# Kernel tuning notes

Hardware: AMD Instinct MI355X
Metric: run time of the kernel (lower is better)

Reference implementation:

```python
import jax, jax.numpy as jnp
import numpy as np

STRIDE = (1, 1)
PAD = (1, 1)
DIL = (1, 1)
KH, KW = 3, 3
DEFORM_GROUPS = 2


def setup_inputs() -> dict:
    key = jax.random.key(0)
    ks = jax.random.split(key, 5)
    B, C, H, W = 4, 128, 64, 64
    Cout = 128
    K = KH * KW
    n = C * KH * KW
    stdv = 1.0 / np.sqrt(n)
    x = jax.random.normal(ks[0], (B, C, H, W), dtype=jnp.float32)
    offset = jax.random.normal(ks[1], (B, DEFORM_GROUPS * 2 * K, H, W), dtype=jnp.float32)
    mask = jax.random.uniform(ks[2], (B, DEFORM_GROUPS * K, H, W), dtype=jnp.float32)
    weight = jax.random.uniform(ks[3], (Cout, C, KH, KW), minval=-stdv, maxval=stdv, dtype=jnp.float32)
    bias = jnp.zeros((Cout,), dtype=jnp.float32)
    return {"x": x, "offset": offset, "mask": mask, "weight": weight, "bias": bias}


def _mdcn_forward(x, offset, mask, weight, bias):
    B, C, H, W = x.shape
    Cout, Cin_g, kh, kw = weight.shape
    K = kh * kw
    dg = offset.shape[1] // (2 * K)
    Cg = C // dg
    sh, sw = STRIDE
    ph, pw = PAD
    dh, dw = DIL
    Ho = (H + 2 * ph - (dh * (kh - 1) + 1)) // sh + 1
    Wo = (W + 2 * pw - (dw * (kw - 1) + 1)) // sw + 1

    # offsets: (B, dg, K, 2, Ho, Wo) with (dy, dx) pairs; mask: (B, dg, K, Ho, Wo)
    off = offset.reshape(B, dg, K, 2, Ho, Wo)
    m = mask.reshape(B, dg, K, Ho, Wo)

    ky, kx = jnp.meshgrid(jnp.arange(kh), jnp.arange(kw), indexing="ij")
    ky = ky.reshape(K).astype(x.dtype)  # kernel tap row offsets
    kx = kx.reshape(K).astype(x.dtype)
    oy = (jnp.arange(Ho) * sh - ph).astype(x.dtype)
    ox = (jnp.arange(Wo) * sw - pw).astype(x.dtype)

    # sampling positions (B, dg, K, Ho, Wo)
    py = off[:, :, :, 0] + oy[None, None, None, :, None] + (ky * dh)[None, None, :, None, None]
    px = off[:, :, :, 1] + ox[None, None, None, None, :] + (kx * dw)[None, None, :, None, None]

    y0 = jnp.floor(py)
    x0 = jnp.floor(px)
    ly = py - y0
    lx = px - x0
    y0i = y0.astype(jnp.int32)
    x0i = x0.astype(jnp.int32)

    xg = x.reshape(B, dg, Cg, H * W)

    def gather(yi, xi):
        valid = (yi >= 0) & (yi < H) & (xi >= 0) & (xi < W)
        idx = jnp.clip(yi, 0, H - 1) * W + jnp.clip(xi, 0, W - 1)  # (B,dg,K,Ho,Wo)
        g = jax.vmap(jax.vmap(lambda xf, ix: xf[:, ix]))(xg, idx.reshape(B, dg, K * Ho * Wo))
        g = g.reshape(B, dg, Cg, K, Ho, Wo)
        return g * valid[:, :, None].astype(x.dtype)

    w00 = ((1 - ly) * (1 - lx))[:, :, None]
    w01 = ((1 - ly) * lx)[:, :, None]
    w10 = (ly * (1 - lx))[:, :, None]
    w11 = (ly * lx)[:, :, None]

    val = (w00 * gather(y0i, x0i)
           + w01 * gather(y0i, x0i + 1)
           + w10 * gather(y0i + 1, x0i)
           + w11 * gather(y0i + 1, x0i + 1))

    # modulation and im2col-GEMM (groups=1): col (B, C*K, Ho*Wo)
    col = (val * m[:, :, None]).reshape(B, C * K, Ho * Wo)
    wk = weight.reshape(Cout, C * K)
    out = jnp.einsum("ok,bkp->bop", wk, col).reshape(B, Cout, Ho, Wo)
    return out + bias[None, :, None, None]


def reference(x, offset, mask, weight, bias):
    return _mdcn_forward(x, offset, mask, weight, bias)
```

## Files before the change

kernel.cpp:

```cpp
#include <hip/hip_runtime.h>
#include <hip/hip_fp16.h>

#define B_    4
#define C_    128
#define H_    64
#define W_    64
#define CO_   128
#define K_    9
#define DG_   2
#define HW_   4096
#define CK_   1152
#define NKT_  36
#define NPAIR_ 576
#define XSTR_ 68

typedef __attribute__((ext_vector_type(8))) short    short8;
typedef __attribute__((ext_vector_type(4))) float    floatx4;
typedef __attribute__((ext_vector_type(4))) _Float16 h4v;

__device__ __align__(16) unsigned short g_wA[NKT_ * 8 * 64 * 8];
__device__ __align__(16) unsigned int   g_colu[(size_t)B_ * 64 * NPAIR_ * 64];
__device__ __align__(16) int4           g_desc[B_ * DG_ * K_ * HW_];

__device__ __forceinline__ unsigned short f32_to_bf16(float f) {
    unsigned int u = __float_as_uint(f);
    u += 0x7FFFu + ((u >> 16) & 1u);
    return (unsigned short)(u >> 16);
}
__device__ __forceinline__ unsigned int pack_bf16x2(float a, float b) {
    return (unsigned int)f32_to_bf16(a) | ((unsigned int)f32_to_bf16(b) << 16);
}

__global__ __launch_bounds__(256) void prep_kernel(
    const float* __restrict__ w,
    const float* __restrict__ offset,
    const float* __restrict__ mask)
{
    const int bid = blockIdx.x;
    if (bid < 576) {
        const int lin  = bid * 256 + threadIdx.x;
        const int j    = lin & 7;
        const int lane = (lin >> 3) & 63;
        const int mtkt = lin >> 9;
        const int mt   = mtkt & 7;
        const int kt   = mtkt >> 3;
        const int co   = mt * 16 + (lane & 15);
        const int kp   = kt * 32 + (lane >> 4) * 8 + j;
        const int c    = kp & 127;
        const int k    = kp >> 7;
        g_wA[lin] = f32_to_bf16(w[co * CK_ + c * 9 + k]);
    } else {
        const int lin = (bid - 576) * 256 + threadIdx.x;
        const int pix = lin & (HW_ - 1);
        const int bgk = lin >> 12;
        const int k   = bgk % 9;
        const int bg  = bgk / 9;
        const int ho = pix >> 6;
        const int wo = pix & 63;
        const int ky = k / 3;
        const int kx = k - 3 * ky;

        const float py = offset[(size_t)(bg * 18 + 2 * k)     * HW_ + pix] + (float)(ho - 1 + ky);
        const float px = offset[(size_t)(bg * 18 + 2 * k + 1) * HW_ + pix] + (float)(wo - 1 + kx);
        const float m  = mask  [(size_t)(bg * 9 + k)          * HW_ + pix];

        const float y0f = floorf(py);
        const float x0f = floorf(px);
        const float ly = py - y0f;
        const float lx = px - x0f;
        const int y0 = (int)y0f;
        const int x0 = (int)x0f;

        const bool yin = (y0 >= 0) & (y0 <= H_ - 2);
        const float er0 = yin ? (1.0f - ly) : ((y0 == -1)     ? ly          : 0.0f);
        const float er1 = yin ? ly          : ((y0 == H_ - 1) ? (1.0f - ly) : 0.0f);
        const bool xin = (x0 >= 0) & (x0 <= W_ - 2);
        const float ec0 = xin ? (1.0f - lx) : ((x0 == -1)     ? lx          : 0.0f);
        const float ec1 = xin ? lx          : ((x0 == W_ - 1) ? (1.0f - lx) : 0.0f);
        const int yc = min(max(y0, 0), H_ - 2);
        const int xc = min(max(x0, 0), W_ - 2);

        const __half2 wlo = __floats2half2_rn(m * er0 * ec0, m * er0 * ec1);
        const __half2 whi = __floats2half2_rn(m * er1 * ec0, m * er1 * ec1);
        int4 d;
        d.x = yc * XSTR_ + xc;
        d.y = __builtin_bit_cast(int, wlo);
        d.z = __builtin_bit_cast(int, whi);
        d.w = 0;
        g_desc[lin] = d;
    }
}

__global__ __launch_bounds__(1024) void col_kernel(const float* __restrict__ x)
{
    const int bid = blockIdx.x;
    const int b   = bid >> 7;
    const int rem = bid & 127;
    const int cq  = rem >> 2;
    const int qu  = rem & 3;
    const int c0  = cq * 4;
    const int g   = cq >> 4;
    const int t   = threadIdx.x;

    __shared__ h4v s_x4[64 * XSTR_];

    {
        const int p0  = t * 4;
        const int row = p0 >> 6;
        const int col = p0 & 63;
        const float* __restrict__ src = x + ((size_t)(b * C_ + c0) << 12) + p0;
        const float4 f0 = *(const float4*)(src);
        const float4 f1 = *(const float4*)(src + HW_);
        const float4 f2 = *(const float4*)(src + 2 * HW_);
        const float4 f3 = *(const float4*)(src + 3 * HW_);
        h4v* dst = s_x4 + row * XSTR_ + col;
        dst[0] = h4v{(_Float16)f0.x, (_Float16)f1.x, (_Float16)f2.x, (_Float16)f3.x};
        dst[1] = h4v{(_Float16)f0.y, (_Float16)f1.y, (_Float16)f2.y, (_Float16)f3.y};
        dst[2] = h4v{(_Float16)f0.z, (_Float16)f1.z, (_Float16)f2.z, (_Float16)f3.z};
        dst[3] = h4v{(_Float16)f0.w, (_Float16)f1.w, (_Float16)f2.w, (_Float16)f3.w};
    }
    __syncthreads();

    const int pix = qu * 1024 + t;
    const int pt  = pix >> 6;
    const int pl  = pix & 63;
    const int4* __restrict__ descb =
        g_desc + (size_t)((b * DG_ + g) * 9) * HW_ + pix;
    unsigned int* __restrict__ outb =
        g_colu + ((size_t)(b * 64 + pt) * NPAIR_ + 2 * cq) * 64 + pl;

#pragma unroll
    for (int k = 0; k < 9; ++k) {
        const int4 d = descb[(size_t)k * HW_];
        const float2 wl = __half22float2(__builtin_bit_cast(__half2, d.y));
        const float2 wh = __half22float2(__builtin_bit_cast(__half2, d.z));
        const h4v* p = s_x4 + d.x;
        const h4v lo0 = p[0];
        const h4v lo1 = p[1];
        const h4v hi0 = p[XSTR_];
        const h4v hi1 = p[XSTR_ + 1];
        float v[4];
#pragma unroll
        for (int ci = 0; ci < 4; ++ci)
            v[ci] = wl.x * (float)lo0[ci] + wl.y * (float)lo1[ci]
                  + wh.x * (float)hi0[ci] + wh.y * (float)hi1[ci];
        outb[k * 64 * 64]      = pack_bf16x2(v[0], v[1]);
        outb[k * 64 * 64 + 64] = pack_bf16x2(v[2], v[3]);
    }
}

__global__ __launch_bounds__(1024) void gemm_kernel(
    const float* __restrict__ bias, float* __restrict__ out)
{
    const int bid  = blockIdx.x;
    const int b    = bid >> 6;
    const int pt   = bid & 63;
    const int t    = threadIdx.x;
    const int w    = t >> 6;
    const int cw   = w >> 2;
    const int nt   = w & 3;
    const int lane = t & 63;
    const int l15  = lane & 15;
    const int quad = lane >> 4;

    const unsigned short* __restrict__ ap = g_wA + ((size_t)(cw * 2) * 64 + lane) * 8;
    const unsigned int* __restrict__ bp =
        g_colu + ((size_t)(b * 64 + pt) * NPAIR_ + quad * 4) * 64 + nt * 16 + l15;

    floatx4 acc0 = {0.f, 0.f, 0.f, 0.f};
    floatx4 acc1 = {0.f, 0.f, 0.f, 0.f};

    short8 a0c = *(const short8*)ap;
    short8 a1c = *(const short8*)(ap + 512);
    uint4 u0;
    u0.x = bp[0]; u0.y = bp[64]; u0.z = bp[128]; u0.w = bp[192];
    short8 b_c = __builtin_bit_cast(short8, u0);

#pragma unroll 4
    for (int kt = 0; kt < NKT_; ++kt) {
        short8 a0n = a0c, a1n = a1c, b_n = b_c;
        if (kt < NKT_ - 1) {
            const unsigned short* an = ap + (size_t)(kt + 1) * 4096;
            a0n = *(const short8*)an;
            a1n = *(const short8*)(an + 512);
            const unsigned int* bq = bp + (size_t)(kt + 1) * 1024;
            uint4 u;
            u.x = bq[0]; u.y = bq[64]; u.z = bq[128]; u.w = bq[192];
            b_n = __builtin_bit_cast(short8, u);
        }
        acc0 = __builtin_amdgcn_mfma_f32_16x16x32_bf16(a0c, b_c, acc0, 0, 0, 0);
        acc1 = __builtin_amdgcn_mfma_f32_16x16x32_bf16(a1c, b_c, acc1, 0, 0, 0);
        a0c = a0n; a1c = a1n; b_c = b_n;
    }

    const int pixo = pt * 64 + nt * 16 + l15;
#pragma unroll
    for (int mtl = 0; mtl < 2; ++mtl) {
        const floatx4 a = mtl ? acc1 : acc0;
        const int cob = cw * 32 + mtl * 16 + quad * 4;
#pragma unroll
        for (int r = 0; r < 4; ++r) {
            const int co = cob + r;
            out[((size_t)(b * CO_ + co) << 12) + pixo] = a[r] + bias[co];
        }
    }
}

extern "C" void kernel_launch(void* const* d_in, const int* in_sizes, int n_in,
                              void* d_out, int out_size, void* d_ws, size_t ws_size,
                              hipStream_t stream) {
    const float* x      = (const float*)d_in[0];
    const float* offset = (const float*)d_in[1];
    const float* mask   = (const float*)d_in[2];
    const float* weight = (const float*)d_in[3];
    const float* bias   = (const float*)d_in[4];
    float* out = (float*)d_out;

    hipLaunchKernelGGL(prep_kernel, dim3(576 + 1152), dim3(256), 0, stream, weight, offset, mask);
    hipLaunchKernelGGL(col_kernel, dim3(512), dim3(1024), 0, stream, x);
    hipLaunchKernelGGL(gemm_kernel, dim3(256), dim3(1024), 0, stream, bias, out);
}
```

Measured before the change: 100.3 us.

## Pack column buffer as 4-channel uint2 and use hardware conversions

```diff
diff --git a/kernel.cpp b/kernel.cpp
--- a/kernel.cpp
+++ b/kernel.cpp
@@ -1,5 +1,6 @@
 #include <hip/hip_runtime.h>
 #include <hip/hip_fp16.h>
+#include <hip/hip_bf16.h>
 
 #define B_    4
 #define C_    128
@@ -11,15 +12,20 @@
 #define HW_   4096
 #define CK_   1152
 #define NKT_  36
-#define NPAIR_ 576
+#define NQP_  288
 #define XSTR_ 68
 
 typedef __attribute__((ext_vector_type(8))) short    short8;
 typedef __attribute__((ext_vector_type(4))) float    floatx4;
+typedef __attribute__((ext_vector_type(2))) _Float16 h2v;
 typedef __attribute__((ext_vector_type(4))) _Float16 h4v;
 
+__device__ __forceinline__ h2v pkrtz(float a, float b) {
+    return __builtin_bit_cast(h2v, __builtin_amdgcn_cvt_pkrtz(a, b));
+}
+
 __device__ __align__(16) unsigned short g_wA[NKT_ * 8 * 64 * 8];
-__device__ __align__(16) unsigned int   g_colu[(size_t)B_ * 64 * NPAIR_ * 64];
+__device__ __align__(16) uint2          g_colq[(size_t)B_ * 64 * NQP_ * 64];
 __device__ __align__(16) int4           g_desc[B_ * DG_ * K_ * HW_];
 
 __device__ __forceinline__ unsigned short f32_to_bf16(float f) {
@@ -27,8 +33,10 @@
     u += 0x7FFFu + ((u >> 16) & 1u);
     return (unsigned short)(u >> 16);
 }
-__device__ __forceinline__ unsigned int pack_bf16x2(float a, float b) {
-    return (unsigned int)f32_to_bf16(a) | ((unsigned int)f32_to_bf16(b) << 16);
+__device__ __forceinline__ unsigned int pack_bf16x2_hw(float a, float b) {
+    union { __hip_bfloat162 h; unsigned int u; } cvt;
+    cvt.h = __float22bfloat162_rn(make_float2(a, b));
+    return cvt.u;
 }
 
 __global__ __launch_bounds__(256) void prep_kernel(
@@ -82,10 +90,12 @@
 
         const __half2 wlo = __floats2half2_rn(m * er0 * ec0, m * er0 * ec1);
         const __half2 whi = __floats2half2_rn(m * er1 * ec0, m * er1 * ec1);
+        union { __half2 h; int i; } ulo, uhi;
+        ulo.h = wlo; uhi.h = whi;
         int4 d;
         d.x = yc * XSTR_ + xc;
-        d.y = __builtin_bit_cast(int, wlo);
-        d.z = __builtin_bit_cast(int, whi);
+        d.y = ulo.i;
+        d.z = uhi.i;
         d.w = 0;
         g_desc[lin] = d;
     }
@@ -114,10 +124,10 @@
         const float4 f2 = *(const float4*)(src + 2 * HW_);
         const float4 f3 = *(const float4*)(src + 3 * HW_);
         h4v* dst = s_x4 + row * XSTR_ + col;
-        dst[0] = h4v{(_Float16)f0.x, (_Float16)f1.x, (_Float16)f2.x, (_Float16)f3.x};
-        dst[1] = h4v{(_Float16)f0.y, (_Float16)f1.y, (_Float16)f2.y, (_Float16)f3.y};
-        dst[2] = h4v{(_Float16)f0.z, (_Float16)f1.z, (_Float16)f2.z, (_Float16)f3.z};
-        dst[3] = h4v{(_Float16)f0.w, (_Float16)f1.w, (_Float16)f2.w, (_Float16)f3.w};
+        dst[0] = __builtin_shufflevector(pkrtz(f0.x, f1.x), pkrtz(f2.x, f3.x), 0, 1, 2, 3);
+        dst[1] = __builtin_shufflevector(pkrtz(f0.y, f1.y), pkrtz(f2.y, f3.y), 0, 1, 2, 3);
+        dst[2] = __builtin_shufflevector(pkrtz(f0.z, f1.z), pkrtz(f2.z, f3.z), 0, 1, 2, 3);
+        dst[3] = __builtin_shufflevector(pkrtz(f0.w, f1.w), pkrtz(f2.w, f3.w), 0, 1, 2, 3);
     }
     __syncthreads();
 
@@ -126,26 +136,34 @@
     const int pl  = pix & 63;
     const int4* __restrict__ descb =
         g_desc + (size_t)((b * DG_ + g) * 9) * HW_ + pix;
-    unsigned int* __restrict__ outb =
-        g_colu + ((size_t)(b * 64 + pt) * NPAIR_ + 2 * cq) * 64 + pl;
+    uint2* __restrict__ outb =
+        g_colq + ((size_t)(b * 64 + pt) * NQP_ + cq) * 64 + pl;
+
+    int4 d[9];
+#pragma unroll
+    for (int k = 0; k < 9; ++k) d[k] = descb[(size_t)k * HW_];
 
 #pragma unroll
     for (int k = 0; k < 9; ++k) {
-        const int4 d = descb[(size_t)k * HW_];
-        const float2 wl = __half22float2(__builtin_bit_cast(__half2, d.y));
-        const float2 wh = __half22float2(__builtin_bit_cast(__half2, d.z));
-        const h4v* p = s_x4 + d.x;
+        const h2v wl = __builtin_bit_cast(h2v, d[k].y);
+        const h2v wh = __builtin_bit_cast(h2v, d[k].z);
+        const h4v* p = s_x4 + d[k].x;
         const h4v lo0 = p[0];
         const h4v lo1 = p[1];
         const h4v hi0 = p[XSTR_];
         const h4v hi1 = p[XSTR_ + 1];
         float v[4];
 #pragma unroll
-        for (int ci = 0; ci < 4; ++ci)
-            v[ci] = wl.x * (float)lo0[ci] + wl.y * (float)lo1[ci]
-                  + wh.x * (float)hi0[ci] + wh.y * (float)hi1[ci];
-        outb[k * 64 * 64]      = pack_bf16x2(v[0], v[1]);
-        outb[k * 64 * 64 + 64] = pack_bf16x2(v[2], v[3]);
+        for (int ci = 0; ci < 4; ++ci) {
+            float a;
+            a = (float)wl[0] * (float)lo0[ci];
+            a = fmaf((float)wl[1], (float)lo1[ci], a);
+            a = fmaf((float)wh[0], (float)hi0[ci], a);
+            a = fmaf((float)wh[1], (float)hi1[ci], a);
+            v[ci] = a;
+        }
+        outb[(size_t)k * 32 * 64] = make_uint2(pack_bf16x2_hw(v[0], v[1]),
+                                               pack_bf16x2_hw(v[2], v[3]));
     }
 }
 
@@ -164,16 +182,16 @@
     const int quad = lane >> 4;
 
     const unsigned short* __restrict__ ap = g_wA + ((size_t)(cw * 2) * 64 + lane) * 8;
-    const unsigned int* __restrict__ bp =
-        g_colu + ((size_t)(b * 64 + pt) * NPAIR_ + quad * 4) * 64 + nt * 16 + l15;
+    const uint2* __restrict__ bp =
+        g_colq + ((size_t)(b * 64 + pt) * NQP_ + quad * 2) * 64 + nt * 16 + l15;
 
     floatx4 acc0 = {0.f, 0.f, 0.f, 0.f};
     floatx4 acc1 = {0.f, 0.f, 0.f, 0.f};
 
     short8 a0c = *(const short8*)ap;
     short8 a1c = *(const short8*)(ap + 512);
-    uint4 u0;
-    u0.x = bp[0]; u0.y = bp[64]; u0.z = bp[128]; u0.w = bp[192];
+    uint2 ua = bp[0], ub = bp[64];
+    uint4 u0 = make_uint4(ua.x, ua.y, ub.x, ub.y);
     short8 b_c = __builtin_bit_cast(short8, u0);
 
 #pragma unroll 4
@@ -183,10 +201,9 @@
             const unsigned short* an = ap + (size_t)(kt + 1) * 4096;
             a0n = *(const short8*)an;
             a1n = *(const short8*)(an + 512);
-            const unsigned int* bq = bp + (size_t)(kt + 1) * 1024;
-            uint4 u;
-            u.x = bq[0]; u.y = bq[64]; u.z = bq[128]; u.w = bq[192];
-            b_n = __builtin_bit_cast(short8, u);
+            const uint2* bq = bp + (size_t)(kt + 1) * 512;
+            const uint2 va = bq[0], vb = bq[64];
+            b_n = __builtin_bit_cast(short8, make_uint4(va.x, va.y, vb.x, vb.y));
         }
         acc0 = __builtin_amdgcn_mfma_f32_16x16x32_bf16(a0c, b_c, acc0, 0, 0, 0);
         acc1 = __builtin_amdgcn_mfma_f32_16x16x32_bf16(a1c, b_c, acc1, 0, 0, 0);
```

New measurement: 103.4 us. 1.03x slower.
